# Performance work log

Hardware: AMD Instinct MI355X
Metric: run time of the kernel (lower is better)

The kernel has to match this reference:

```python
import jax, jax.numpy as jnp
import numpy as np

BATCH_SIZE = 1024  # init kwarg: Pair(batch_size)
D = 260            # per-item feature dim; last 4 entries are (x1, y1, x2, y2)


def setup_inputs() -> dict:
    key = jax.random.key(0)
    k_feat, k_xy, k_wh = jax.random.split(key, 3)
    feats = jax.random.normal(k_feat, (1, BATCH_SIZE, D - 4), dtype=jnp.float32)
    # Valid boxes: x2 > x1, y2 > y1 so areas are strictly positive (avoids div-by-zero,
    # matching the intended use on real detector boxes).
    xy1 = jax.random.uniform(k_xy, (1, BATCH_SIZE, 2), minval=0.0, maxval=0.5)
    wh = jax.random.uniform(k_wh, (1, BATCH_SIZE, 2), minval=0.05, maxval=0.5)
    bbox = jnp.concatenate([xy1, xy1 + wh], axis=-1)  # (x1, y1, x2, y2)
    inputs = jnp.concatenate([feats, bbox], axis=-1).astype(jnp.float32)
    return {"inputs": inputs}


def reference(inputs) -> jnp.ndarray:
    n = inputs.shape[1] // 2          # loops run over range(batch_size // 2)
    d = inputs.shape[2]
    x = inputs[0, :n]                 # [n, D] — only first half of rows is used
    x1, y1, x2, y2 = x[:, -4], x[:, -3], x[:, -2], x[:, -1]
    area = (x2 - x1) * (y2 - y1)      # [n]
    # Pairwise intersection, all (i, j) at once.
    w = jnp.maximum(0.0, jnp.minimum(x2[:, None], x2[None, :]) - jnp.maximum(x1[:, None], x1[None, :]))
    h = jnp.maximum(0.0, jnp.minimum(y2[:, None], y2[None, :]) - jnp.maximum(y1[:, None], y1[None, :]))
    inter = w * h                     # [n, n]
    r1 = inter / area[:, None]        # intersection / area_i
    r2 = inter / area[None, :]        # intersection / area_j
    xi = jnp.broadcast_to(x[:, None, :], (n, n, d))  # features of i
    xj = jnp.broadcast_to(x[None, :, :], (n, n, d))  # features of j
    out = jnp.concatenate([xi, xj, r1[..., None], r2[..., None]], axis=-1)  # [n, n, 2D+2]
    # Original appends in i-outer, j-inner order then concats on axis 1.
    return out.reshape(1, n * n, 2 * d + 2)
```

## Files before the change

kernel.cpp:

```cpp
#include <hip/hip_runtime.h>


#define NPAIR 512
#define DFEAT 260
#define ROW_OUT2 261

__global__ __launch_bounds__(256) void pair_kernel(const float* __restrict__ in,
                                                   float* __restrict__ out) {
    const int p = blockIdx.x;
    const int i = p >> 9;
    const int j = p & (NPAIR - 1);

    const float* rowi = in + (size_t)i * DFEAT;
    const float* rowj = in + (size_t)j * DFEAT;

    const float x1i = rowi[256], y1i = rowi[257], x2i = rowi[258], y2i = rowi[259];
    const float x1j = rowj[256], y1j = rowj[257], x2j = rowj[258], y2j = rowj[259];

    float w = fminf(x2i, x2j) - fmaxf(x1i, x1j);
    float h = fminf(y2i, y2j) - fmaxf(y1i, y1j);
    w = fmaxf(w, 0.0f);
    h = fmaxf(h, 0.0f);
    const float inter = w * h;
    const float area_i = (x2i - x1i) * (y2i - y1i);
    const float area_j = (x2j - x1j) * (y2j - y1j);
    const float r1 = inter / area_i;
    const float r2 = inter / area_j;

    const float2* rowi2 = (const float2*)rowi;
    const float2* rowj2 = (const float2*)rowj;
    float2* orow = (float2*)(out + (size_t)p * 522);

    for (int t = threadIdx.x; t < ROW_OUT2; t += 256) {
        float2 v;
        if (t < 130) {
            v = rowi2[t];
        } else if (t < 260) {
            v = rowj2[t - 130];
        } else {
            v = make_float2(r1, r2);
        }
        orow[t] = v;
    }
}

extern "C" void kernel_launch(void* const* d_in, const int* in_sizes, int n_in,
                              void* d_out, int out_size, void* d_ws, size_t ws_size,
                              hipStream_t stream) {
    const float* in = (const float*)d_in[0];
    float* out = (float*)d_out;
    pair_kernel<<<NPAIR * NPAIR, 256, 0, stream>>>(in, out);
}
```

Baseline: 629.2 us.

## Process 64 pairs per block with flat float4 output writes

```diff
diff --git a/kernel.cpp b/kernel.cpp
--- a/kernel.cpp
+++ b/kernel.cpp
@@ -1,46 +1,65 @@
 #include <hip/hip_runtime.h>
 
 
-#define NPAIR 512
-#define DFEAT 260
-#define ROW_OUT2 261
+#define N 512
+#define D 260
+#define ROW 522
+#define JT 64
+#define SPAN (JT * ROW)
+#define SPAN4 (SPAN / 4)
 
 __global__ __launch_bounds__(256) void pair_kernel(const float* __restrict__ in,
                                                    float* __restrict__ out) {
-    const int p = blockIdx.x;
-    const int i = p >> 9;
-    const int j = p & (NPAIR - 1);
+    const int bi = blockIdx.x;
+    const int i  = bi >> 3;
+    const int j0 = (bi & 7) * JT;
 
-    const float* rowi = in + (size_t)i * DFEAT;
-    const float* rowj = in + (size_t)j * DFEAT;
+    __shared__ float s_r1[JT];
+    __shared__ float s_r2[JT];
 
-    const float x1i = rowi[256], y1i = rowi[257], x2i = rowi[258], y2i = rowi[259];
-    const float x1j = rowj[256], y1j = rowj[257], x2j = rowj[258], y2j = rowj[259];
+    const int tid = threadIdx.x;
 
-    float w = fminf(x2i, x2j) - fmaxf(x1i, x1j);
-    float h = fminf(y2i, y2j) - fmaxf(y1i, y1j);
-    w = fmaxf(w, 0.0f);
-    h = fmaxf(h, 0.0f);
-    const float inter = w * h;
-    const float area_i = (x2i - x1i) * (y2i - y1i);
-    const float area_j = (x2j - x1j) * (y2j - y1j);
-    const float r1 = inter / area_i;
-    const float r2 = inter / area_j;
+    if (tid < JT) {
+        const float* bi_ = in + (size_t)i * D + 256;
+        const float* bj_ = in + (size_t)(j0 + tid) * D + 256;
+        const float x1i = bi_[0], y1i = bi_[1], x2i = bi_[2], y2i = bi_[3];
+        const float x1j = bj_[0], y1j = bj_[1], x2j = bj_[2], y2j = bj_[3];
+        float w = fminf(x2i, x2j) - fmaxf(x1i, x1j);
+        float h = fminf(y2i, y2j) - fmaxf(y1i, y1j);
+        w = fmaxf(w, 0.0f);
+        h = fmaxf(h, 0.0f);
+        const float inter  = w * h;
+        const float area_i = (x2i - x1i) * (y2i - y1i);
+        const float area_j = (x2j - x1j) * (y2j - y1j);
+        s_r1[tid] = inter / area_i;
+        s_r2[tid] = inter / area_j;
+    }
+    __syncthreads();
 
-    const float2* rowi2 = (const float2*)rowi;
-    const float2* rowj2 = (const float2*)rowj;
-    float2* orow = (float2*)(out + (size_t)p * 522);
+    const float* rowi = in + (size_t)i * D;
+    float4* ospan = (float4*)(out + (size_t)bi * SPAN);
 
-    for (int t = threadIdx.x; t < ROW_OUT2; t += 256) {
-        float2 v;
-        if (t < 130) {
-            v = rowi2[t];
-        } else if (t < 260) {
-            v = rowj2[t - 130];
-        } else {
-            v = make_float2(r1, r2);
+    for (int f = tid; f < SPAN4; f += 256) {
+        const int e0 = f * 4;
+        float v[4];
+#pragma unroll
+        for (int k = 0; k < 4; ++k) {
+            const unsigned e  = (unsigned)(e0 + k);
+            const unsigned lj = e / 522u;
+            const unsigned c  = e - lj * 522u;
+            float val;
+            if (c < 260u) {
+                val = rowi[c];
+            } else if (c < 520u) {
+                val = in[(size_t)(j0 + lj) * D + (c - 260u)];
+            } else if (c == 520u) {
+                val = s_r1[lj];
+            } else {
+                val = s_r2[lj];
+            }
+            v[k] = val;
         }
-        orow[t] = v;
+        ospan[f] = make_float4(v[0], v[1], v[2], v[3]);
     }
 }
 
@@ -49,5 +68,5 @@
                               hipStream_t stream) {
     const float* in = (const float*)d_in[0];
     float* out = (float*)d_out;
-    pair_kernel<<<NPAIR * NPAIR, 256, 0, stream>>>(in, out);
+    pair_kernel<<<N * (N / JT), 256, 0, stream>>>(in, out);
 }
```

Result: faster. 583.2 us (-7.3%).

## Tile pairs per block with shared-memory j rows and per-wave row writes

Applied to the files above, without the earlier changes.

```diff
diff --git a/kernel.cpp b/kernel.cpp
--- a/kernel.cpp
+++ b/kernel.cpp
@@ -1,46 +1,61 @@
 #include <hip/hip_runtime.h>
 
 
-#define NPAIR 512
-#define DFEAT 260
-#define ROW_OUT2 261
+#define N 512
+#define D 260
+#define JT 32
 
 __global__ __launch_bounds__(256) void pair_kernel(const float* __restrict__ in,
                                                    float* __restrict__ out) {
-    const int p = blockIdx.x;
-    const int i = p >> 9;
-    const int j = p & (NPAIR - 1);
+    const int b    = blockIdx.x;
+    const int i    = b >> 4;
+    const int j0   = (b & 15) * JT;
+    const int tid  = threadIdx.x;
+    const int lane = tid & 63;
+    const int w    = tid >> 6;
 
-    const float* rowi = in + (size_t)i * DFEAT;
-    const float* rowj = in + (size_t)j * DFEAT;
+    __shared__ float2 s_xj[JT * 130];
+    __shared__ float  s_r1[JT], s_r2[JT];
 
-    const float x1i = rowi[256], y1i = rowi[257], x2i = rowi[258], y2i = rowi[259];
-    const float x1j = rowj[256], y1j = rowj[257], x2j = rowj[258], y2j = rowj[259];
+    const float* rowi = in + i * D;
+    const float2 xi_a = *(const float2*)(rowi + 2 * lane);
+    const float2 xi_b = *(const float2*)(rowi + 128 + 2 * lane);
+    const float4 bb   = *(const float4*)(rowi + 256);
 
-    float w = fminf(x2i, x2j) - fmaxf(x1i, x1j);
-    float h = fminf(y2i, y2j) - fmaxf(y1i, y1j);
-    w = fmaxf(w, 0.0f);
-    h = fmaxf(h, 0.0f);
-    const float inter = w * h;
-    const float area_i = (x2i - x1i) * (y2i - y1i);
-    const float area_j = (x2j - x1j) * (y2j - y1j);
-    const float r1 = inter / area_i;
-    const float r2 = inter / area_j;
+    const float2* gj2 = (const float2*)(in + (size_t)j0 * D);
+    for (int t = tid; t < JT * 130; t += 256) s_xj[t] = gj2[t];
 
-    const float2* rowi2 = (const float2*)rowi;
-    const float2* rowj2 = (const float2*)rowj;
-    float2* orow = (float2*)(out + (size_t)p * 522);
+    if (tid < JT) {
+        const float* bj = in + (size_t)(j0 + tid) * D + 256;
+        const float x1j = bj[0], y1j = bj[1], x2j = bj[2], y2j = bj[3];
+        const float x1i = bb.x, y1i = bb.y, x2i = bb.z, y2i = bb.w;
+        float ww = fmaxf(0.0f, fminf(x2i, x2j) - fmaxf(x1i, x1j));
+        float hh = fmaxf(0.0f, fminf(y2i, y2j) - fmaxf(y1i, y1j));
+        const float inter = ww * hh;
+        s_r1[tid] = inter / ((x2i - x1i) * (y2i - y1i));
+        s_r2[tid] = inter / ((x2j - x1j) * (y2j - y1j));
+    }
+    __syncthreads();
 
-    for (int t = threadIdx.x; t < ROW_OUT2; t += 256) {
-        float2 v;
-        if (t < 130) {
-            v = rowi2[t];
-        } else if (t < 260) {
-            v = rowj2[t - 130];
-        } else {
-            v = make_float2(r1, r2);
+    for (int lj = w; lj < JT; lj += 4) {
+        float2* ob = (float2*)(out + (size_t)(i * N + j0 + lj) * 522);
+        const float2* xr = &s_xj[lj * 130];
+
+        const int idx2 = (lane < 2) ? 0 : (lane - 2);
+        float2 v2 = xr[idx2];
+        if (lane == 0) v2 = make_float2(bb.x, bb.y);
+        if (lane == 1) v2 = make_float2(bb.z, bb.w);
+        const float2 v3 = xr[62 + lane];
+
+        ob[lane]       = xi_a;
+        ob[64 + lane]  = xi_b;
+        ob[128 + lane] = v2;
+        ob[192 + lane] = v3;
+        if (lane < 5) {
+            const float2 v4 = (lane < 4) ? xr[126 + ((lane < 4) ? lane : 3)]
+                                         : make_float2(s_r1[lj], s_r2[lj]);
+            ob[256 + lane] = v4;
         }
-        orow[t] = v;
     }
 }
 
@@ -49,5 +64,5 @@
                               hipStream_t stream) {
     const float* in = (const float*)d_in[0];
     float* out = (float*)d_out;
-    pair_kernel<<<NPAIR * NPAIR, 256, 0, stream>>>(in, out);
+    pair_kernel<<<N * (N / JT), 256, 0, stream>>>(in, out);
 }
```

New measurement: 536.7 us. 14.7% less time.
